# Kernel tuning notes

Measured on AMD Instinct MI355X. Metric: run time of the kernel, lower is better.

Reference implementation:

```python
import jax, jax.numpy as jnp
import numpy as np

NUM_GROUPS = 32
EPS = 1e-05
HT_MIN = -1.0
HT_MAX = 1.0


def setup_inputs() -> dict:
    key = jax.random.key(0)
    k1, k2, k3 = jax.random.split(key, 3)
    B, IN, OUT = 4096, 2048, 2048
    x = jax.random.normal(k1, (B, IN), dtype=jnp.float32)
    # kaiming-uniform-ish scale for weight, uniform bias bound 1/sqrt(in)
    weight = jax.random.normal(k2, (OUT, IN), dtype=jnp.float32) * (1.0 / np.sqrt(IN))
    bias = jax.random.uniform(k3, (OUT,), dtype=jnp.float32, minval=-1.0 / np.sqrt(IN), maxval=1.0 / np.sqrt(IN))
    gn_weight = jnp.ones((OUT,), dtype=jnp.float32)
    gn_bias = jnp.zeros((OUT,), dtype=jnp.float32)
    return {"x": x, "weight": weight, "bias": bias, "gn_weight": gn_weight, "gn_bias": gn_bias}


def reference(x, weight, bias, gn_weight, gn_bias):
    # Linear: y = x @ W^T + b   -> [B, OUT]
    y = jnp.einsum("bi,oi->bo", x, weight) + bias
    B, C = y.shape
    G = NUM_GROUPS
    yg = y.reshape(B, G, C // G)
    mean = jnp.mean(yg, axis=-1, keepdims=True)
    var = jnp.mean(jnp.square(yg), axis=-1, keepdims=True) - jnp.square(mean)
    yn = ((yg - mean) * jax.lax.rsqrt(var + EPS)).reshape(B, C)
    out = yn * gn_weight + gn_bias
    return jnp.clip(out, HT_MIN, HT_MAX)
```

## Files before the change

### kernel.cpp

```cpp
#include <hip/hip_runtime.h>
#include <stdint.h>

#define B_ROWS 4096
#define C_OUT  2048
#define C_IN   2048
#define EPS    1e-5f

typedef __attribute__((ext_vector_type(8))) short bf16x8;
typedef __attribute__((ext_vector_type(4))) float f32x4;

__device__ __forceinline__ unsigned short f2bf(float f) {
    uint32_t u = __float_as_uint(f);
    uint32_t r = (u + 0x7fffu + ((u >> 16) & 1u)) >> 16;
    return (unsigned short)r;
}

__global__ void cvt_f32_bf16_kernel(const float* __restrict__ x,
                                    const float* __restrict__ w,
                                    unsigned short* __restrict__ xb,
                                    unsigned short* __restrict__ wb,
                                    int nx4, int nw4) {
    int i = blockIdx.x * blockDim.x + threadIdx.x;
    const float* src;
    unsigned short* dst;
    if (i < nx4) {
        src = x; dst = xb;
    } else {
        i -= nx4;
        if (i >= nw4) return;
        src = w; dst = wb;
    }
    float4 v = ((const float4*)src)[i];
    ushort4 o;
    o.x = f2bf(v.x); o.y = f2bf(v.y); o.z = f2bf(v.z); o.w = f2bf(v.w);
    ((ushort4*)dst)[i] = o;
}

__global__ __launch_bounds__(256, 3)
void gemm_gn_kernel(const unsigned short* __restrict__ A,
                    const unsigned short* __restrict__ W,
                    const float* __restrict__ bias,
                    const float* __restrict__ gnw,
                    const float* __restrict__ gnb,
                    float* __restrict__ out) {
    __shared__ __align__(16) unsigned short smem[2 * 12288];

    const int flat = blockIdx.x;
    const int br   = (flat >> 4) & 31;
    const int bc   = (flat & 15) | ((flat >> 9) << 4);
    const int t    = threadIdx.x;
    const int lane = t & 63;
    const int wave = t >> 6;
    const int wr   = wave & 1;
    const int kh   = wave >> 1;
    const int c16  = lane & 15;
    const int quad = lane >> 4;

    f32x4 acc[4][4];
#pragma unroll
    for (int i = 0; i < 4; i++)
#pragma unroll
        for (int j = 0; j < 4; j++) acc[i][j] = (f32x4){0.f, 0.f, 0.f, 0.f};

    const int r0 = t >> 3;
    const int qo = ((t & 7) ^ (r0 & 7)) * 8;
    const unsigned short* gA = A + (size_t)(br * 128 + r0) * C_IN + qo;
    const unsigned short* gB = W + (size_t)(bc * 64 + r0) * C_IN + qo;

    const int qs = (((kh << 2) | quad) ^ (c16 & 7)) * 8;

#define STAGE(buf, k0)                                                                     \
    do {                                                                                   \
        unsigned short* sa = smem + (buf) * 12288;                                         \
        unsigned short* sb = sa + 8192;                                                    \
        _Pragma("unroll")                                                                  \
        for (int n = 0; n < 4; n++)                                                        \
            __builtin_amdgcn_global_load_lds(                                              \
                (const __attribute__((address_space(1))) void*)(gA + (size_t)(n * 32) * C_IN + (k0)), \
                (__attribute__((address_space(3))) void*)(sa + n * 2048 + t * 8), 16, 0, 0); \
        _Pragma("unroll")                                                                  \
        for (int n = 0; n < 2; n++)                                                        \
            __builtin_amdgcn_global_load_lds(                                              \
                (const __attribute__((address_space(1))) void*)(gB + (size_t)(n * 32) * C_IN + (k0)), \
                (__attribute__((address_space(3))) void*)(sb + n * 2048 + t * 8), 16, 0, 0); \
    } while (0)

    STAGE(0, 0);
    int cur = 0;
    for (int it = 0; it < 32; ++it) {
        __syncthreads();
        if (it < 31) STAGE(cur ^ 1, (it + 1) * 64);

        const unsigned short* sa = smem + cur * 12288;
        const unsigned short* sb = sa + 8192;
        bf16x8 a[4], b[4];
#pragma unroll
        for (int i = 0; i < 4; i++)
            a[i] = *(const bf16x8*)(sa + (wr * 64 + i * 16 + c16) * 64 + qs);
#pragma unroll
        for (int j = 0; j < 4; j++)
            b[j] = *(const bf16x8*)(sb + (j * 16 + c16) * 64 + qs);
#pragma unroll
        for (int i = 0; i < 4; i++)
#pragma unroll
            for (int j = 0; j < 4; j++)
                acc[i][j] = __builtin_amdgcn_mfma_f32_16x16x32_bf16(a[i], b[j], acc[i][j], 0, 0, 0);
        cur ^= 1;
    }

    __syncthreads();
    float* fbuf = (float*)smem;
    if (kh == 1) {
#pragma unroll
        for (int i = 0; i < 4; i++)
#pragma unroll
            for (int j = 0; j < 4; j++)
                *(f32x4*)(fbuf + wr * 4096 + i * 1024 + j * 256 + lane * 4) = acc[i][j];
    }
    __syncthreads();
    if (kh == 1) return;
#pragma unroll
    for (int i = 0; i < 4; i++)
#pragma unroll
        for (int j = 0; j < 4; j++)
            acc[i][j] += *(const f32x4*)(fbuf + wr * 4096 + i * 1024 + j * 256 + lane * 4);

    const int colbase = bc * 64;
    const int rowbase = br * 128 + wr * 64;
    float bv[4], gw[4], gb[4];
#pragma unroll
    for (int j = 0; j < 4; j++) {
        int col = colbase + j * 16 + c16;
        bv[j] = bias[col];
        gw[j] = gnw[col];
        gb[j] = gnb[col];
    }
#pragma unroll
    for (int i = 0; i < 4; i++) {
#pragma unroll
        for (int r = 0; r < 4; r++) {
            float s = 0.f, ss = 0.f;
#pragma unroll
            for (int j = 0; j < 4; j++) {
                float v = acc[i][j][r] + bv[j];
                acc[i][j][r] = v;
                s += v;
                ss += v * v;
            }
#pragma unroll
            for (int m = 1; m < 16; m <<= 1) {
                s  += __shfl_xor(s, m, 64);
                ss += __shfl_xor(ss, m, 64);
            }
            float mean = s * (1.f / 64.f);
            float var  = ss * (1.f / 64.f) - mean * mean;
            float rstd = rsqrtf(var + EPS);
            int row = rowbase + i * 16 + quad * 4 + r;
            float* orow = out + (size_t)row * C_OUT;
#pragma unroll
            for (int j = 0; j < 4; j++) {
                float v = (acc[i][j][r] - mean) * rstd * gw[j] + gb[j];
                v = fminf(1.f, fmaxf(-1.f, v));
                orow[colbase + j * 16 + c16] = v;
            }
        }
    }
}

extern "C" void kernel_launch(void* const* d_in, const int* in_sizes, int n_in,
                              void* d_out, int out_size, void* d_ws, size_t ws_size,
                              hipStream_t stream) {
    const float* x    = (const float*)d_in[0];
    const float* w    = (const float*)d_in[1];
    const float* bias = (const float*)d_in[2];
    const float* gnw  = (const float*)d_in[3];
    const float* gnb  = (const float*)d_in[4];
    float* out = (float*)d_out;

    unsigned short* xb = (unsigned short*)d_ws;
    unsigned short* wb = xb + (size_t)B_ROWS * C_IN;

    const int nx4 = B_ROWS * C_IN / 4;
    const int nw4 = C_OUT * C_IN / 4;
    cvt_f32_bf16_kernel<<<(nx4 + nw4 + 255) / 256, 256, 0, stream>>>(x, w, xb, wb, nx4, nw4);

    gemm_gn_kernel<<<1024, 256, 0, stream>>>(xb, wb, bias, gnw, gnb, out);
}
```

Baseline: 151.4 us.

## Enlarge GEMM tile to 128x128 and drop intra-block split-K reduction

```diff
diff --git a/kernel.cpp b/kernel.cpp
--- a/kernel.cpp
+++ b/kernel.cpp
@@ -36,23 +36,22 @@
     ((ushort4*)dst)[i] = o;
 }
 
-__global__ __launch_bounds__(256, 3)
+__global__ __launch_bounds__(256, 2)
 void gemm_gn_kernel(const unsigned short* __restrict__ A,
                     const unsigned short* __restrict__ W,
                     const float* __restrict__ bias,
                     const float* __restrict__ gnw,
                     const float* __restrict__ gnb,
                     float* __restrict__ out) {
-    __shared__ __align__(16) unsigned short smem[2 * 12288];
+    __shared__ __align__(16) unsigned short smem[2 * 16384];
 
-    const int flat = blockIdx.x;
-    const int br   = (flat >> 4) & 31;
-    const int bc   = (flat & 15) | ((flat >> 9) << 4);
+    const int bc   = blockIdx.x;
+    const int br   = blockIdx.y;
     const int t    = threadIdx.x;
     const int lane = t & 63;
     const int wave = t >> 6;
-    const int wr   = wave & 1;
-    const int kh   = wave >> 1;
+    const int wr   = wave >> 1;
+    const int wc   = wave & 1;
     const int c16  = lane & 15;
     const int quad = lane >> 4;
 
@@ -65,13 +64,11 @@
     const int r0 = t >> 3;
     const int qo = ((t & 7) ^ (r0 & 7)) * 8;
     const unsigned short* gA = A + (size_t)(br * 128 + r0) * C_IN + qo;
-    const unsigned short* gB = W + (size_t)(bc * 64 + r0) * C_IN + qo;
-
-    const int qs = (((kh << 2) | quad) ^ (c16 & 7)) * 8;
+    const unsigned short* gB = W + (size_t)(bc * 128 + r0) * C_IN + qo;
 
 #define STAGE(buf, k0)                                                                     \
     do {                                                                                   \
-        unsigned short* sa = smem + (buf) * 12288;                                         \
+        unsigned short* sa = smem + (buf) * 16384;                                         \
         unsigned short* sb = sa + 8192;                                                    \
         _Pragma("unroll")                                                                  \
         for (int n = 0; n < 4; n++)                                                        \
@@ -79,7 +76,7 @@
                 (const __attribute__((address_space(1))) void*)(gA + (size_t)(n * 32) * C_IN + (k0)), \
                 (__attribute__((address_space(3))) void*)(sa + n * 2048 + t * 8), 16, 0, 0); \
         _Pragma("unroll")                                                                  \
-        for (int n = 0; n < 2; n++)                                                        \
+        for (int n = 0; n < 4; n++)                                                        \
             __builtin_amdgcn_global_load_lds(                                              \
                 (const __attribute__((address_space(1))) void*)(gB + (size_t)(n * 32) * C_IN + (k0)), \
                 (__attribute__((address_space(3))) void*)(sb + n * 2048 + t * 8), 16, 0, 0); \
@@ -91,41 +88,28 @@
         __syncthreads();
         if (it < 31) STAGE(cur ^ 1, (it + 1) * 64);
 
-        const unsigned short* sa = smem + cur * 12288;
+        const unsigned short* sa = smem + cur * 16384;
         const unsigned short* sb = sa + 8192;
-        bf16x8 a[4], b[4];
 #pragma unroll
-        for (int i = 0; i < 4; i++)
-            a[i] = *(const bf16x8*)(sa + (wr * 64 + i * 16 + c16) * 64 + qs);
+        for (int sub = 0; sub < 2; sub++) {
+            const int qs = (((sub << 2) | quad) ^ (c16 & 7)) * 8;
+            bf16x8 a[4], b[4];
 #pragma unroll
-        for (int j = 0; j < 4; j++)
-            b[j] = *(const bf16x8*)(sb + (j * 16 + c16) * 64 + qs);
-#pragma unroll
-        for (int i = 0; i < 4; i++)
+            for (int i = 0; i < 4; i++)
+                a[i] = *(const bf16x8*)(sa + (wr * 64 + i * 16 + c16) * 64 + qs);
 #pragma unroll
             for (int j = 0; j < 4; j++)
-                acc[i][j] = __builtin_amdgcn_mfma_f32_16x16x32_bf16(a[i], b[j], acc[i][j], 0, 0, 0);
+                b[j] = *(const bf16x8*)(sb + (wc * 64 + j * 16 + c16) * 64 + qs);
+#pragma unroll
+            for (int i = 0; i < 4; i++)
+#pragma unroll
+                for (int j = 0; j < 4; j++)
+                    acc[i][j] = __builtin_amdgcn_mfma_f32_16x16x32_bf16(a[i], b[j], acc[i][j], 0, 0, 0);
+        }
         cur ^= 1;
     }
 
-    __syncthreads();
-    float* fbuf = (float*)smem;
-    if (kh == 1) {
-#pragma unroll
-        for (int i = 0; i < 4; i++)
-#pragma unroll
-            for (int j = 0; j < 4; j++)
-                *(f32x4*)(fbuf + wr * 4096 + i * 1024 + j * 256 + lane * 4) = acc[i][j];
-    }
-    __syncthreads();
-    if (kh == 1) return;
-#pragma unroll
-    for (int i = 0; i < 4; i++)
-#pragma unroll
-        for (int j = 0; j < 4; j++)
-            acc[i][j] += *(const f32x4*)(fbuf + wr * 4096 + i * 1024 + j * 256 + lane * 4);
-
-    const int colbase = bc * 64;
+    const int colbase = bc * 128 + wc * 64;
     const int rowbase = br * 128 + wr * 64;
     float bv[4], gw[4], gb[4];
 #pragma unroll
@@ -184,5 +168,6 @@
     const int nw4 = C_OUT * C_IN / 4;
     cvt_f32_bf16_kernel<<<(nx4 + nw4 + 255) / 256, 256, 0, stream>>>(x, w, xb, wb, nx4, nw4);
 
-    gemm_gn_kernel<<<1024, 256, 0, stream>>>(xb, wb, bias, gnw, gnb, out);
+    dim3 grid(C_OUT / 128, B_ROWS / 128);
+    gemm_gn_kernel<<<grid, 256, 0, stream>>>(xb, wb, bias, gnw, gnb, out);
 }
```

After: 137.2 us. 1.1x faster.
